# Kernel tuning notes

Hardware: AMD Instinct MI355X
Metric: run time of the kernel (lower is better)

Reference implementation:

```python
import jax, jax.numpy as jnp
import numpy as np

OUTPUT_SIZE = 7
STRIDES = (4, 8, 16, 32)
IMG = 1024.0


def crop_and_resize(image, boxes, box_ind, crop_size):
    """Faithful jax port of tf.image.crop_and_resize (bilinear, extrapolation_value=0).
    image: (B,H,W,C); boxes: (N,4) interpreted as [y1,x1,y2,x2] in *normalized* coords
    (exactly TF's convention -- note the original module feeds [x1,y1,x2,y2]*1/stride here,
    which is a quirk of the source we reproduce faithfully); box_ind: (N,) int32.
    Returns (N, crop_size, crop_size, C)."""
    B, H, W, C = image.shape
    y1, x1, y2, x2 = boxes[:, 0], boxes[:, 1], boxes[:, 2], boxes[:, 3]
    s = jnp.arange(crop_size, dtype=image.dtype)                      # (cs,)
    h_scale = (y2 - y1) * (H - 1) / (crop_size - 1)                   # (N,)
    w_scale = (x2 - x1) * (W - 1) / (crop_size - 1)
    in_y = y1[:, None] * (H - 1) + s[None, :] * h_scale[:, None]      # (N,cs)
    in_x = x1[:, None] * (W - 1) + s[None, :] * w_scale[:, None]      # (N,cs)
    valid_y = (in_y >= 0) & (in_y <= H - 1)
    valid_x = (in_x >= 0) & (in_x <= W - 1)
    fy = jnp.floor(in_y)
    fx = jnp.floor(in_x)
    y0 = jnp.clip(fy, 0, H - 1).astype(jnp.int32)
    yc = jnp.clip(jnp.ceil(in_y), 0, H - 1).astype(jnp.int32)
    x0 = jnp.clip(fx, 0, W - 1).astype(jnp.int32)
    xc = jnp.clip(jnp.ceil(in_x), 0, W - 1).astype(jnp.int32)
    ly = (in_y - fy)[:, :, None, None]                                # (N,cs,1,1)
    lx = (in_x - fx)[:, None, :, None]                                # (N,1,cs,1)
    b = box_ind[:, None, None]                                        # (N,1,1)
    # 4-corner gathers: each (N, cs, cs, C)
    tl = image[b, y0[:, :, None], x0[:, None, :]]
    tr = image[b, y0[:, :, None], xc[:, None, :]]
    bl = image[b, yc[:, :, None], x0[:, None, :]]
    br = image[b, yc[:, :, None], xc[:, None, :]]
    top = tl + (tr - tl) * lx
    bot = bl + (br - bl) * lx
    out = top + (bot - top) * ly
    valid = (valid_y[:, :, None] & valid_x[:, None, :])[..., None]
    return jnp.where(valid, out, jnp.zeros((), image.dtype))


def roi_align(p2, p3, p4, p5, rois):
    coords = rois[:, 1:]                                              # [x1,y1,x2,y2]
    roi_w = coords[:, 2] - coords[:, 0]
    roi_h = coords[:, 3] - coords[:, 1]
    # FPN level assignment: clip(round(4 + log2(sqrt(h*w)/224)), 2, 5)
    lvl = 4.0 + jnp.log2(jnp.sqrt(roi_h * roi_w) / 224.0)
    roi_level = jnp.clip(jnp.round(lvl).astype(jnp.int32), 2, 5)      # (N,)
    box_ind = rois[:, 0].astype(jnp.int32)
    out = None
    for level, fm, stride in zip((2, 3, 4, 5), (p2, p3, p4, p5), STRIDES):
        # Original passes pixel-scaled [x1,y1,x2,y2]/stride straight into
        # crop_and_resize's [y1,x1,y2,x2] normalized slots; we replicate that.
        boxes = coords * (1.0 / stride)
        pooled = crop_and_resize(fm, boxes, box_ind, OUTPUT_SIZE)     # (N,7,7,C)
        sel = (roi_level == level)[:, None, None, None]
        contrib = jnp.where(sel, pooled, jnp.zeros((), pooled.dtype))
        out = contrib if out is None else out + contrib
    # each roi matches exactly one level, so the masked sum equals the original
    # per-level gather + concat + argsort-restore (rois stay in original order)
    return out


def setup_inputs() -> dict:
    key = jax.random.key(0)
    k = jax.random.split(key, 9)
    C = 256
    p2 = jax.random.normal(k[0], (2, 256, 256, C), dtype=jnp.float32)
    p3 = jax.random.normal(k[1], (2, 128, 128, C), dtype=jnp.float32)
    p4 = jax.random.normal(k[2], (2, 64, 64, C), dtype=jnp.float32)
    p5 = jax.random.normal(k[3], (2, 32, 32, C), dtype=jnp.float32)
    N = 1000
    bidx = jax.random.randint(k[4], (N,), 0, 2).astype(jnp.float32)
    x1 = jax.random.uniform(k[5], (N,)) * (IMG - 64.0)
    y1 = jax.random.uniform(k[6], (N,)) * (IMG - 64.0)
    # log-uniform roi sizes in [16, 645] so all FPN levels get hit
    w = 2.0 ** (4.0 + jax.random.uniform(k[7], (N,)) * 5.333)
    h = 2.0 ** (4.0 + jax.random.uniform(k[8], (N,)) * 5.333)
    rois = jnp.stack([bidx, x1, y1,
                      jnp.minimum(x1 + w, IMG),
                      jnp.minimum(y1 + h, IMG)], axis=1).astype(jnp.float32)
    return {"p2": p2, "p3": p3, "p4": p4, "p5": p5, "rois": rois}


def reference(p2, p3, p4, p5, rois):
    return roi_align(p2, p3, p4, p5, rois)
```

## Files before the change

### kernel.cpp

```cpp
#include <hip/hip_runtime.h>


constexpr int CH = 256;

__global__ __launch_bounds__(256)
void roi_align_kernel(const float* __restrict__ p2,
                      const float* __restrict__ p3,
                      const float* __restrict__ p4,
                      const float* __restrict__ p5,
                      const float* __restrict__ rois,
                      float* __restrict__ out,
                      int nrois)
{
#pragma clang fp contract(off)
    int idx = blockIdx.x * blockDim.x + threadIdx.x;
    int total = nrois * 49 * 64;
    if (idx >= total) return;

    int c4   = idx & 63;
    int t    = idx >> 6;
    int n    = t / 49;
    int cell = t - n * 49;
    int i    = cell / 7;
    int j    = cell - i * 7;

    const float* r = rois + n * 5;
    int   b  = (int)r[0];
    float x1 = r[1], y1 = r[2], x2 = r[3], y2 = r[4];

    float rw = x2 - x1, rh = y2 - y1;
    float lvl = 4.0f + log2f(sqrtf(rh * rw) / 224.0f);
    int level = (int)rintf(lvl);
    level = level < 2 ? 2 : (level > 5 ? 5 : level);

    const float* fm; int H; float inv_s;
    if (level == 2)      { fm = p2; H = 256; inv_s = 0.25f;    }
    else if (level == 3) { fm = p3; H = 128; inv_s = 0.125f;   }
    else if (level == 4) { fm = p4; H = 64;  inv_s = 0.0625f;  }
    else                 { fm = p5; H = 32;  inv_s = 0.03125f; }

    float cy1 = x1 * inv_s, cx1 = y1 * inv_s;
    float cy2 = x2 * inv_s, cx2 = y2 * inv_s;
    float Hm1 = (float)(H - 1);
    float h_scale = (cy2 - cy1) * Hm1 / 6.0f;
    float w_scale = (cx2 - cx1) * Hm1 / 6.0f;
    float in_y = cy1 * Hm1 + (float)i * h_scale;
    float in_x = cx1 * Hm1 + (float)j * w_scale;

    float4* op = (float4*)(out + (size_t)(n * 49 + cell) * CH) + c4;

    bool valid = (in_y >= 0.0f) & (in_y <= Hm1) & (in_x >= 0.0f) & (in_x <= Hm1);
    if (!valid) {
        *op = make_float4(0.f, 0.f, 0.f, 0.f);
        return;
    }

    float fy = floorf(in_y), fx = floorf(in_x);
    int y0 = (int)fminf(fmaxf(fy, 0.f), Hm1);
    int yc = (int)fminf(fmaxf(ceilf(in_y), 0.f), Hm1);
    int x0 = (int)fminf(fmaxf(fx, 0.f), Hm1);
    int xc = (int)fminf(fmaxf(ceilf(in_x), 0.f), Hm1);
    float ly = in_y - fy, lx = in_x - fx;

    const float* img = fm + (size_t)b * H * H * CH;
    const float4 vtl = *((const float4*)(img + ((size_t)y0 * H + x0) * CH) + c4);
    const float4 vtr = *((const float4*)(img + ((size_t)y0 * H + xc) * CH) + c4);
    const float4 vbl = *((const float4*)(img + ((size_t)yc * H + x0) * CH) + c4);
    const float4 vbr = *((const float4*)(img + ((size_t)yc * H + xc) * CH) + c4);

    float4 res;
    float top, bot;
    top = vtl.x + (vtr.x - vtl.x) * lx;
    bot = vbl.x + (vbr.x - vbl.x) * lx;
    res.x = top + (bot - top) * ly;
    top = vtl.y + (vtr.y - vtl.y) * lx;
    bot = vbl.y + (vbr.y - vbl.y) * lx;
    res.y = top + (bot - top) * ly;
    top = vtl.z + (vtr.z - vtl.z) * lx;
    bot = vbl.z + (vbr.z - vbl.z) * lx;
    res.z = top + (bot - top) * ly;
    top = vtl.w + (vtr.w - vtl.w) * lx;
    bot = vbl.w + (vbr.w - vbl.w) * lx;
    res.w = top + (bot - top) * ly;

    *op = res;
}

extern "C" void kernel_launch(void* const* d_in, const int* in_sizes, int n_in,
                              void* d_out, int out_size, void* d_ws, size_t ws_size,
                              hipStream_t stream)
{
    const float* p2   = (const float*)d_in[0];
    const float* p3   = (const float*)d_in[1];
    const float* p4   = (const float*)d_in[2];
    const float* p5   = (const float*)d_in[3];
    const float* rois = (const float*)d_in[4];
    float* out = (float*)d_out;

    int nrois = in_sizes[4] / 5;
    int total = nrois * 49 * 64;
    int block = 256;
    int grid  = (total + block - 1) / block;
    roi_align_kernel<<<grid, block, 0, stream>>>(p2, p3, p4, p5, rois, out, nrois);
}
```

Before: 201.8 us.

## Precompute per-ROI parameters in a prepass kernel and use nontemporal stores

Adds a small prepass kernel that computes each ROI's level, scales, offsets and image base once and writes them to workspace. The main kernel then reads two vectors per thread instead of recomputing log2/sqrt and the level selection for every channel group. Output writes now use nontemporal stores to avoid polluting the cache with streaming output. The cost is an extra kernel launch and a dependency on workspace memory.

```diff
diff --git a/kernel.cpp b/kernel.cpp
--- a/kernel.cpp
+++ b/kernel.cpp
@@ -3,14 +3,49 @@
 
 constexpr int CH = 256;
 
+typedef float v4f __attribute__((ext_vector_type(4)));
+
 __global__ __launch_bounds__(256)
-void roi_align_kernel(const float* __restrict__ p2,
-                      const float* __restrict__ p3,
-                      const float* __restrict__ p4,
-                      const float* __restrict__ p5,
-                      const float* __restrict__ rois,
-                      float* __restrict__ out,
-                      int nrois)
+void roi_params_kernel(const float* __restrict__ rois,
+                       v4f* __restrict__ params, int nrois)
+{
+#pragma clang fp contract(off)
+    int n = blockIdx.x * blockDim.x + threadIdx.x;
+    if (n >= nrois) return;
+    const float* r = rois + n * 5;
+    int   b  = (int)r[0];
+    float x1 = r[1], y1 = r[2], x2 = r[3], y2 = r[4];
+
+    float lvl = 4.0f + log2f(sqrtf((y2 - y1) * (x2 - x1)) / 224.0f);
+    int level = (int)rintf(lvl);
+    level = level < 2 ? 2 : (level > 5 ? 5 : level);
+
+    int H; float inv_s;
+    if (level == 2)      { H = 256; inv_s = 0.25f;    }
+    else if (level == 3) { H = 128; inv_s = 0.125f;   }
+    else if (level == 4) { H = 64;  inv_s = 0.0625f;  }
+    else                 { H = 32;  inv_s = 0.03125f; }
+
+    float cy1 = x1 * inv_s, cx1 = y1 * inv_s;
+    float cy2 = x2 * inv_s, cx2 = y2 * inv_s;
+    float Hm1 = (float)(H - 1);
+    float h_scale = (cy2 - cy1) * Hm1 / 6.0f;
+    float w_scale = (cx2 - cx1) * Hm1 / 6.0f;
+
+    v4f pa; pa.x = cy1 * Hm1; pa.y = h_scale; pa.z = cx1 * Hm1; pa.w = w_scale;
+    v4f pb; pb.x = Hm1;
+    pb.y = __int_as_float(H);
+    pb.z = __int_as_float(b * H * H * CH);
+    pb.w = __int_as_float(level);
+    params[n * 2 + 0] = pa;
+    params[n * 2 + 1] = pb;
+}
+
+__global__ __launch_bounds__(256)
+void roi_align_main(const float* __restrict__ p2, const float* __restrict__ p3,
+                    const float* __restrict__ p4, const float* __restrict__ p5,
+                    const v4f* __restrict__ params,
+                    float* __restrict__ out, int nrois)
 {
 #pragma clang fp contract(off)
     int idx = blockIdx.x * blockDim.x + threadIdx.x;
@@ -24,36 +59,26 @@
     int i    = cell / 7;
     int j    = cell - i * 7;
 
-    const float* r = rois + n * 5;
-    int   b  = (int)r[0];
-    float x1 = r[1], y1 = r[2], x2 = r[3], y2 = r[4];
+    v4f pa = params[n * 2 + 0];
+    v4f pb = params[n * 2 + 1];
 
-    float rw = x2 - x1, rh = y2 - y1;
-    float lvl = 4.0f + log2f(sqrtf(rh * rw) / 224.0f);
-    int level = (int)rintf(lvl);
-    level = level < 2 ? 2 : (level > 5 ? 5 : level);
+    float in_y = pa.x + (float)i * pa.y;
+    float in_x = pa.z + (float)j * pa.w;
+    float Hm1  = pb.x;
 
-    const float* fm; int H; float inv_s;
-    if (level == 2)      { fm = p2; H = 256; inv_s = 0.25f;    }
-    else if (level == 3) { fm = p3; H = 128; inv_s = 0.125f;   }
-    else if (level == 4) { fm = p4; H = 64;  inv_s = 0.0625f;  }
-    else                 { fm = p5; H = 32;  inv_s = 0.03125f; }
-
-    float cy1 = x1 * inv_s, cx1 = y1 * inv_s;
-    float cy2 = x2 * inv_s, cx2 = y2 * inv_s;
-    float Hm1 = (float)(H - 1);
-    float h_scale = (cy2 - cy1) * Hm1 / 6.0f;
-    float w_scale = (cx2 - cx1) * Hm1 / 6.0f;
-    float in_y = cy1 * Hm1 + (float)i * h_scale;
-    float in_x = cx1 * Hm1 + (float)j * w_scale;
-
-    float4* op = (float4*)(out + (size_t)(n * 49 + cell) * CH) + c4;
+    v4f* op = (v4f*)out + idx;
 
     bool valid = (in_y >= 0.0f) & (in_y <= Hm1) & (in_x >= 0.0f) & (in_x <= Hm1);
     if (!valid) {
-        *op = make_float4(0.f, 0.f, 0.f, 0.f);
+        v4f z; z.x = 0.f; z.y = 0.f; z.z = 0.f; z.w = 0.f;
+        __builtin_nontemporal_store(z, op);
         return;
     }
+
+    int H       = __float_as_int(pb.y);
+    int img_off = __float_as_int(pb.z);
+    int level   = __float_as_int(pb.w);
+    const float* fm = level == 2 ? p2 : level == 3 ? p3 : level == 4 ? p4 : p5;
 
     float fy = floorf(in_y), fx = floorf(in_x);
     int y0 = (int)fminf(fmaxf(fy, 0.f), Hm1);
@@ -62,28 +87,20 @@
     int xc = (int)fminf(fmaxf(ceilf(in_x), 0.f), Hm1);
     float ly = in_y - fy, lx = in_x - fx;
 
-    const float* img = fm + (size_t)b * H * H * CH;
-    const float4 vtl = *((const float4*)(img + ((size_t)y0 * H + x0) * CH) + c4);
-    const float4 vtr = *((const float4*)(img + ((size_t)y0 * H + xc) * CH) + c4);
-    const float4 vbl = *((const float4*)(img + ((size_t)yc * H + x0) * CH) + c4);
-    const float4 vbr = *((const float4*)(img + ((size_t)yc * H + xc) * CH) + c4);
+    const float* img = fm + img_off;
+    const v4f vtl = *((const v4f*)(img + ((size_t)y0 * H + x0) * CH) + c4);
+    const v4f vtr = *((const v4f*)(img + ((size_t)y0 * H + xc) * CH) + c4);
+    const v4f vbl = *((const v4f*)(img + ((size_t)yc * H + x0) * CH) + c4);
+    const v4f vbr = *((const v4f*)(img + ((size_t)yc * H + xc) * CH) + c4);
 
-    float4 res;
-    float top, bot;
-    top = vtl.x + (vtr.x - vtl.x) * lx;
-    bot = vbl.x + (vbr.x - vbl.x) * lx;
-    res.x = top + (bot - top) * ly;
-    top = vtl.y + (vtr.y - vtl.y) * lx;
-    bot = vbl.y + (vbr.y - vbl.y) * lx;
-    res.y = top + (bot - top) * ly;
-    top = vtl.z + (vtr.z - vtl.z) * lx;
-    bot = vbl.z + (vbr.z - vbl.z) * lx;
-    res.z = top + (bot - top) * ly;
-    top = vtl.w + (vtr.w - vtl.w) * lx;
-    bot = vbl.w + (vbr.w - vbl.w) * lx;
-    res.w = top + (bot - top) * ly;
-
-    *op = res;
+    v4f res;
+    {
+        v4f top, bot;
+        top = vtl + (vtr - vtl) * lx;
+        bot = vbl + (vbr - vbl) * lx;
+        res = top + (bot - top) * ly;
+    }
+    __builtin_nontemporal_store(res, op);
 }
 
 extern "C" void kernel_launch(void* const* d_in, const int* in_sizes, int n_in,
@@ -96,10 +113,13 @@
     const float* p5   = (const float*)d_in[3];
     const float* rois = (const float*)d_in[4];
     float* out = (float*)d_out;
+    v4f* params = (v4f*)d_ws;
 
     int nrois = in_sizes[4] / 5;
+
+    roi_params_kernel<<<(nrois + 255) / 256, 256, 0, stream>>>(rois, params, nrois);
+
     int total = nrois * 49 * 64;
-    int block = 256;
-    int grid  = (total + block - 1) / block;
-    roi_align_kernel<<<grid, block, 0, stream>>>(p2, p3, p4, p5, rois, out, nrois);
+    roi_align_main<<<(total + 255) / 256, 256, 0, stream>>>(p2, p3, p4, p5,
+                                                            params, out, nrois);
 }
```

Measured after the change: 197.5 us. 1.02x faster.
